# Optimization experiments

Hardware: AMD Instinct MI355X
Metric: run time of the kernel (lower is better)

The kernel has to match this reference:

```python
import jax, jax.numpy as jnp
import numpy as np

ROPE_THETA = 10000.0


def apply_rope(q, k, cos, sin):
    # q,k: [B,H,S,D]; cos,sin: [S,D/2] -> broadcast [1,1,S,D/2]
    def rot(t):
        t2 = t.reshape(*t.shape[:-1], -1, 2)  # [B,H,S,D/2,2]
        te, to = t2[..., 0], t2[..., 1]
        c = cos[None, None, :, :]
        s = sin[None, None, :, :]
        re = te * c - to * s
        im = te * s + to * c
        return jnp.stack([re, im], axis=-1).reshape(t.shape)
    return rot(q), rot(k)


def setup_inputs() -> dict:
    key = jax.random.key(0)
    ks = jax.random.split(key, 4)
    B, S, D, H = 2, 2048, 1024, 16
    hd = D // H
    x = jax.random.normal(ks[0], (B, S, D), dtype=jnp.float32)
    # causal boolean mask (True = keep)
    mask = jnp.tril(jnp.ones((S, S), dtype=bool))[None, None]
    # rotary tables
    inv_freq = 1.0 / (ROPE_THETA ** (jnp.arange(0, hd, 2, dtype=jnp.float32) / hd))  # [hd/2]
    t = jnp.arange(S, dtype=jnp.float32)
    ang = t[:, None] * inv_freq[None, :]  # [S, hd/2]
    freqs_cos = jnp.cos(ang)
    freqs_sin = jnp.sin(ang)
    W_qkv = jax.random.normal(ks[1], (D, 3 * D), dtype=jnp.float32) * 0.02
    b_qkv = jnp.zeros((3 * D,), dtype=jnp.float32)
    W_o = jax.random.normal(ks[2], (D, D), dtype=jnp.float32) * 0.02
    b_o = jnp.zeros((D,), dtype=jnp.float32)
    return {"x": x, "mask": mask, "freqs_cos": freqs_cos, "freqs_sin": freqs_sin,
            "W_qkv": W_qkv, "b_qkv": b_qkv, "W_o": W_o, "b_o": b_o}


def reference(x, mask, freqs_cos, freqs_sin, W_qkv, b_qkv, W_o, b_o):
    B, S, D = x.shape
    H = 16
    hd = D // H
    scale = hd ** -0.5
    qkv = x @ W_qkv + b_qkv  # [B,S,3D]
    q, k, v = jnp.split(qkv, 3, axis=-1)
    q = q.reshape(B, S, H, hd).transpose(0, 2, 1, 3)  # [B,H,S,hd]
    k = k.reshape(B, S, H, hd).transpose(0, 2, 1, 3)
    v = v.reshape(B, S, H, hd).transpose(0, 2, 1, 3)
    q, k = apply_rope(q, k, freqs_cos, freqs_sin)
    scores = jnp.einsum('bhqd,bhkd->bhqk', q, k) * scale
    scores = jnp.where(mask, scores, jnp.finfo(scores.dtype).min)
    attn = jax.nn.softmax(scores, axis=-1)
    out = jnp.einsum('bhqk,bhkd->bhqd', attn, v)
    out = out.transpose(0, 2, 1, 3).reshape(B, S, D)
    return out @ W_o + b_o
```

## Files before the change

kernel.cpp:

```cpp
#include <hip/hip_runtime.h>
#include <hip/hip_bf16.h>
#include <stdint.h>

typedef unsigned short u16;
typedef __attribute__((ext_vector_type(8))) __bf16 bf16x8;
typedef __attribute__((ext_vector_type(4))) float f32x4;
typedef __attribute__((ext_vector_type(16))) float f32x16;
typedef __attribute__((ext_vector_type(8))) u16 u16x8;

__device__ __forceinline__ u16 f2bf(float f) {
  union { float f; unsigned int u; } v; v.f = f;
  unsigned int r = v.u + 0x7fffu + ((v.u >> 16) & 1u);
  return (u16)(r >> 16);
}
__device__ __forceinline__ unsigned pack2(float lo, float hi) {
  return (unsigned)f2bf(lo) | ((unsigned)f2bf(hi) << 16);
}

__device__ __forceinline__ f32x4 mfma16(bf16x8 a, bf16x8 b, f32x4 c) {
  return __builtin_amdgcn_mfma_f32_16x16x32_bf16(a, b, c, 0, 0, 0);
}
__device__ __forceinline__ f32x16 mfma32(bf16x8 a, bf16x8 b, f32x16 c) {
  return __builtin_amdgcn_mfma_f32_32x32x16_bf16(a, b, c, 0, 0, 0);
}

__device__ __forceinline__ void gload16(const void* g, void* l) {
  __builtin_amdgcn_global_load_lds((const __attribute__((address_space(1))) void*)g,
                                   (__attribute__((address_space(3))) void*)l,
                                   16, 0, 0);
}

__global__ void cast_bf16_kernel(const float* __restrict__ in, u16* __restrict__ out, int n) {
  int i = (blockIdx.x * 256 + threadIdx.x) * 8;
  if (i >= n) return;
  const float4* p = (const float4*)(in + i);
  float4 a = p[0], b = p[1];
  u16x8 o;
  o[0] = f2bf(a.x); o[1] = f2bf(a.y); o[2] = f2bf(a.z); o[3] = f2bf(a.w);
  o[4] = f2bf(b.x); o[5] = f2bf(b.y); o[6] = f2bf(b.z); o[7] = f2bf(b.w);
  *(u16x8*)(out + i) = o;
}

__global__ void transpose_cast_k(const float* __restrict__ in, u16* __restrict__ out,
                                 int R, int Ccols) {
  __shared__ float tile[64][65];
  const int c0 = (int)blockIdx.x << 6, r0 = (int)blockIdx.y << 6;
  const int tx = threadIdx.x & 63, ty = threadIdx.x >> 6;
#pragma unroll
  for (int i = ty; i < 64; i += 4)
    tile[i][tx] = in[(size_t)(r0 + i) * Ccols + c0 + tx];
  __syncthreads();
#pragma unroll
  for (int i = ty; i < 64; i += 4)
    out[(size_t)(c0 + i) * R + r0 + tx] = f2bf(tile[tx][i]);
}

__global__ __launch_bounds__(256, 3)
void gemm_qkv(const u16* __restrict__ A, const u16* __restrict__ Bt,
              const float* __restrict__ bias,
              const float* __restrict__ fc, const float* __restrict__ fs,
              u16* __restrict__ qr, u16* __restrict__ kr, u16* __restrict__ vr) {
  const int K = 1024;
  __shared__ __align__(16) u16 smem[128 * 136];
  u16* const As = smem;
  u16* const Bs = smem + 8192;
  const int m0 = (int)(blockIdx.x / 24) << 7;
  const int n0 = (int)(blockIdx.x % 24) << 7;
  const int tid = threadIdx.x;
  const int l = tid & 63, lg = l >> 4, ll = l & 15;
  const int w = tid >> 6;
  const int wr = (w >> 1) << 6, wc = (w & 1) << 6;
  const int srow = tid >> 2, scol = (tid & 3) << 3;
  const u16* ga = A + (size_t)(m0 + srow) * K + scol;
  const u16* gb = Bt + (size_t)(n0 + srow) * K + scol;
  const size_t K64 = (size_t)64 * K;
  u16* const la00 = &As[srow * 32 + scol];
  u16* const la01 = &As[4096 + srow * 32 + scol];
  u16* const la10 = &As[(srow + 64) * 32 + scol];
  u16* const la11 = &As[4096 + (srow + 64) * 32 + scol];
  u16* const lb00 = &Bs[srow * 32 + scol];
  u16* const lb01 = &Bs[4096 + srow * 32 + scol];
  u16* const lb10 = &Bs[(srow + 64) * 32 + scol];
  u16* const lb11 = &Bs[4096 + (srow + 64) * 32 + scol];
  f32x4 acc[4][4] = {};
  for (int kt = 0; kt < K; kt += 64) {
    gload16(ga + kt, la00);       gload16(ga + kt + 32, la01);
    gload16(ga + kt + K64, la10); gload16(ga + kt + K64 + 32, la11);
    gload16(gb + kt, lb00);       gload16(gb + kt + 32, lb01);
    gload16(gb + kt + K64, lb10); gload16(gb + kt + K64 + 32, lb11);
    __syncthreads();
#pragma unroll
    for (int h = 0; h < 2; ++h) {
      bf16x8 a[4], b[4];
#pragma unroll
      for (int i = 0; i < 4; ++i) {
        a[i] = *(const bf16x8*)&As[h * 4096 + (wr + i * 16 + ll) * 32 + lg * 8];
        b[i] = *(const bf16x8*)&Bs[h * 4096 + (wc + i * 16 + ll) * 32 + lg * 8];
      }
#pragma unroll
      for (int mi = 0; mi < 4; ++mi)
#pragma unroll
        for (int ni = 0; ni < 4; ++ni)
          acc[mi][ni] = mfma16(a[mi], b[ni], acc[mi][ni]);
    }
    __syncthreads();
  }
  const int sec = n0 >> 10;
  u16* const dst = (sec == 0) ? qr : (sec == 1) ? kr : vr;
  const int h0 = (n0 & 1023) >> 6;
#pragma unroll
  for (int ni = 0; ni < 4; ++ni) {
    const int cc = wc + ni * 16 + ll;
    const int n = n0 + cc;
    const int d = n & 63;
    const float bi_ = bias[n];
    const int i2 = d >> 1;
    const bool odd = d & 1;
#pragma unroll
    for (int mi = 0; mi < 4; ++mi) {
#pragma unroll
      for (int r = 0; r < 4; ++r) {
        const int rr = wr + mi * 16 + lg * 4 + r;
        const int s = (m0 + rr) & 2047;
        float v = acc[mi][ni][r] + bi_;
        if (sec < 2) {
          const float c = fc[s * 32 + i2], sn = fs[s * 32 + i2];
          const float p = __shfl_xor(v, 1);
          v = odd ? (p * sn + v * c) : (v * c - p * sn);
          if (sec == 0) v *= 0.125f;
        }
        smem[rr * 136 + cc] = f2bf(v);
      }
    }
  }
  __syncthreads();
#pragma unroll
  for (int it = 0; it < 8; ++it) {
    const int c = it * 256 + tid;
    const int j = c & 7, hh = (c >> 3) & 1, rr = c >> 4;
    const int row = m0 + rr;
    const int bb = row >> 11, ss = row & 2047;
    const uint4 val = *(const uint4*)&smem[rr * 136 + hh * 64 + j * 8];
    *(uint4*)&dst[((size_t)(((bb << 4) + h0 + hh) << 11) + ss) * 64 + j * 8] = val;
  }
}

__global__ __launch_bounds__(256, 2)
void gemm_bt(const u16* __restrict__ A, const u16* __restrict__ Bt,
             const float* __restrict__ bias, float* __restrict__ C,
             int M, int N, int K) {
  __shared__ __align__(16) u16 As[2 * 128 * 32];
  __shared__ __align__(16) u16 Bs[2 * 128 * 32];
  const int nb = N >> 7;
  const int m0 = (int)(blockIdx.x / nb) << 7;
  const int n0 = (int)(blockIdx.x % nb) << 7;
  const int tid = threadIdx.x;
  const int l = tid & 63, lg = l >> 4, ll = l & 15;
  const int w = tid >> 6;
  const int wr = (w >> 1) << 6, wc = (w & 1) << 6;
  const int srow = tid >> 2, scol = (tid & 3) << 3;
  const u16* ga = A + (size_t)(m0 + srow) * K + scol;
  const u16* gb = Bt + (size_t)(n0 + srow) * K + scol;
  const size_t K64 = (size_t)64 * K;
  u16* const la00 = &As[srow * 32 + scol];
  u16* const la01 = &As[4096 + srow * 32 + scol];
  u16* const la10 = &As[(srow + 64) * 32 + scol];
  u16* const la11 = &As[4096 + (srow + 64) * 32 + scol];
  u16* const lb00 = &Bs[srow * 32 + scol];
  u16* const lb01 = &Bs[4096 + srow * 32 + scol];
  u16* const lb10 = &Bs[(srow + 64) * 32 + scol];
  u16* const lb11 = &Bs[4096 + (srow + 64) * 32 + scol];
  f32x4 acc[4][4] = {};
  for (int kt = 0; kt < K; kt += 64) {
    gload16(ga + kt, la00);       gload16(ga + kt + 32, la01);
    gload16(ga + kt + K64, la10); gload16(ga + kt + K64 + 32, la11);
    gload16(gb + kt, lb00);       gload16(gb + kt + 32, lb01);
    gload16(gb + kt + K64, lb10); gload16(gb + kt + K64 + 32, lb11);
    __syncthreads();
#pragma unroll
    for (int h = 0; h < 2; ++h) {
      bf16x8 a[4], b[4];
#pragma unroll
      for (int i = 0; i < 4; ++i) {
        a[i] = *(const bf16x8*)&As[h * 4096 + (wr + i * 16 + ll) * 32 + lg * 8];
        b[i] = *(const bf16x8*)&Bs[h * 4096 + (wc + i * 16 + ll) * 32 + lg * 8];
      }
#pragma unroll
      for (int mi = 0; mi < 4; ++mi)
#pragma unroll
        for (int ni = 0; ni < 4; ++ni)
          acc[mi][ni] = mfma16(a[mi], b[ni], acc[mi][ni]);
    }
    __syncthreads();
  }
#pragma unroll
  for (int mi = 0; mi < 4; ++mi) {
#pragma unroll
    for (int r = 0; r < 4; ++r) {
      const int row = m0 + wr + mi * 16 + lg * 4 + r;
      float* crow = C + (size_t)row * N + n0 + wc;
#pragma unroll
      for (int ni = 0; ni < 4; ++ni)
        crow[ni * 16 + ll] = acc[mi][ni][r] + bias[n0 + wc + ni * 16 + ll];
    }
  }
}

__global__ void v_transpose_bf16(const u16* __restrict__ vr, u16* __restrict__ vtc) {
  __shared__ u16 tile[64][66];
  const int bh = blockIdx.x;
  const int s0 = (int)blockIdx.y << 6;
  const int tx = threadIdx.x & 63, ty = threadIdx.x >> 6;
#pragma unroll
  for (int i = ty; i < 64; i += 4)
    tile[i][tx] = vr[((size_t)bh * 2048 + s0 + i) * 64 + tx];
  __syncthreads();
  u16* const outc = vtc + ((size_t)bh * 32 + (s0 >> 6)) * 4096;
#pragma unroll
  for (int i = ty; i < 64; i += 4)
    outc[i * 64 + tx] = tile[tx][i];
}

__global__ __launch_bounds__(256, 2)
void attn_k(const u16* __restrict__ qr, const u16* __restrict__ kr,
            const u16* __restrict__ vtc, u16* __restrict__ aout) {
  __shared__ __align__(16) char kvlds[16384];
  const int bi = (int)blockIdx.x;
  const int bh = bi & 31;
  const int qt = (bi < 256) ? (15 - (bi >> 5)) : ((bi - 256) >> 5);
  const int tid = threadIdx.x;
  const int w = tid >> 6, l = tid & 63, hi = l >> 5, ql = l & 31;
  const u16* Q  = qr + (size_t)bh * (2048 * 64);
  const u16* Kp = kr + (size_t)bh * (2048 * 64);
  const int q0w = (qt << 7) + (w << 5);
  const int qg = q0w + ql;
  bf16x8 qf[4];
#pragma unroll
  for (int mi = 0; mi < 4; ++mi)
    qf[mi] = *(const bf16x8*)&Q[(size_t)qg * 64 + mi * 16 + hi * 8];
  const int sr = tid >> 2, sc = (tid & 3) * 32;
  const int wo0 = (sr * 128 + sc) ^ ((sr & 7) << 4);
  const int wo1 = (sr * 128 + sc + 16) ^ ((sr & 7) << 4);
  const char* kga = (const char*)(Kp + (size_t)sr * 64) + sc;
  const char* vga = (const char*)(vtc + (size_t)bh * 32 * 4096) + sr * 128 + sc;
  const int swz = (ql & 7) << 4;
  f32x16 oa = {}, ob = {};
  float mrow = -1e30f, lp = 0.f;
  const int nch = 2 * qt + 2;
  uint4 sk0 = *(const uint4*)(kga), sk1 = *(const uint4*)(kga + 16);
  uint4 sv0 = *(const uint4*)(vga), sv1 = *(const uint4*)(vga + 16);
  for (int ch = 0; ch < nch; ++ch) {
    asm volatile("s_waitcnt vmcnt(0)" ::: "memory");
    asm volatile("s_barrier" ::: "memory");
    *(uint4*)(kvlds + wo0) = sk0;
    *(uint4*)(kvlds + wo1) = sk1;
    *(uint4*)(kvlds + 8192 + wo0) = sv0;
    *(uint4*)(kvlds + 8192 + wo1) = sv1;
    if (ch + 1 < nch) {
      const size_t kof = (size_t)(ch + 1) * 8192;
      sk0 = *(const uint4*)(kga + kof); sk1 = *(const uint4*)(kga + kof + 16);
      sv0 = *(const uint4*)(vga + kof); sv1 = *(const uint4*)(vga + kof + 16);
    }
    asm volatile("s_waitcnt lgkmcnt(0)" ::: "memory");
    asm volatile("s_barrier" ::: "memory");
    const int kb = ch << 6;
    if (kb > q0w + 31) continue;
    f32x16 s0 = {}, s1 = {};
#pragma unroll
    for (int mi = 0; mi < 4; ++mi) {
      const int cb = mi * 32 + hi * 16;
      const bf16x8 k0 = *(const bf16x8*)(kvlds + ((ql * 128 + cb) ^ swz));
      const bf16x8 k1 = *(const bf16x8*)(kvlds + (((32 + ql) * 128 + cb) ^ swz));
      s0 = mfma32(k0, qf[mi], s0);
      s1 = mfma32(k1, qf[mi], s1);
    }
    if (kb + 63 > q0w) {
#pragma unroll
      for (int r = 0; r < 16; ++r) {
        const int kvo = (r & 3) + 8 * (r >> 2) + 4 * hi;
        if (kb + kvo > qg) s0[r] = -1e30f;
        if (kb + 32 + kvo > qg) s1[r] = -1e30f;
      }
    }
    float mx = s0[0];
#pragma unroll
    for (int r = 1; r < 16; ++r) mx = fmaxf(mx, s0[r]);
#pragma unroll
    for (int r = 0; r < 16; ++r) mx = fmaxf(mx, s1[r]);
    mx = fmaxf(mx, __shfl_xor(mx, 32));
    if (!__all(mx <= mrow + 8.f)) {
      const float mn = fmaxf(mrow, mx);
      const float esc = __expf(mrow - mn);
      mrow = mn;
      lp *= esc;
#pragma unroll
      for (int r = 0; r < 16; ++r) { oa[r] *= esc; ob[r] *= esc; }
    }
    float p0[16], p1[16];
#pragma unroll
    for (int r = 0; r < 16; ++r) {
      p0[r] = __expf(s0[r] - mrow);
      p1[r] = __expf(s1[r] - mrow);
      lp += p0[r] + p1[r];
    }
    bf16x8 pb[4];
#pragma unroll
    for (int s = 0; s < 2; ++s) {
      const float* ps = s ? p1 : p0;
#pragma unroll
      for (int j = 0; j < 2; ++j) {
        const unsigned X0 = pack2(ps[j * 8 + 0], ps[j * 8 + 1]);
        const unsigned X1 = pack2(ps[j * 8 + 2], ps[j * 8 + 3]);
        const unsigned Y0 = pack2(ps[j * 8 + 4], ps[j * 8 + 5]);
        const unsigned Y1 = pack2(ps[j * 8 + 6], ps[j * 8 + 7]);
        const unsigned sX0 = (unsigned)__shfl_xor((int)X0, 32);
        const unsigned sX1 = (unsigned)__shfl_xor((int)X1, 32);
        const unsigned sY0 = (unsigned)__shfl_xor((int)Y0, 32);
        const unsigned sY1 = (unsigned)__shfl_xor((int)Y1, 32);
        union { unsigned u[4]; bf16x8 v; } t;
        t.u[0] = hi ? sY0 : X0;
        t.u[1] = hi ? sY1 : X1;
        t.u[2] = hi ? Y0 : sX0;
        t.u[3] = hi ? Y1 : sX1;
        pb[s * 2 + j] = t.v;
      }
    }
#pragma unroll
    for (int jj = 0; jj < 4; ++jj) {
      const int cb = jj * 32 + hi * 16;
      const bf16x8 va = *(const bf16x8*)(kvlds + 8192 + ((ql * 128 + cb) ^ swz));
      const bf16x8 vb = *(const bf16x8*)(kvlds + 8192 + (((32 + ql) * 128 + cb) ^ swz));
      oa = mfma32(va, pb[jj], oa);
      ob = mfma32(vb, pb[jj], ob);
    }
  }
  lp += __shfl_xor(lp, 32);
  const float inv = 1.0f / lp;
  const int hcol = (bh & 15) << 6;
  const int tok = ((bh >> 4) << 11) + qg;
  unsigned* orow = (unsigned*)(aout + (size_t)tok * 1024 + hcol);
#pragma unroll
  for (int r = 0; r < 16; r += 2) {
    const int d0 = (r & 3) + 8 * (r >> 2) + 4 * hi;
    orow[d0 >> 1]        = pack2(oa[r] * inv, oa[r + 1] * inv);
    orow[(32 + d0) >> 1] = pack2(ob[r] * inv, ob[r + 1] * inv);
  }
}

extern "C" void kernel_launch(void* const* d_in, const int* in_sizes, int n_in,
                              void* d_out, int out_size, void* d_ws, size_t ws_size,
                              hipStream_t stream) {
  const float* x    = (const float*)d_in[0];
  const float* fc   = (const float*)d_in[2];
  const float* fs   = (const float*)d_in[3];
  const float* Wqkv = (const float*)d_in[4];
  const float* bqkv = (const float*)d_in[5];
  const float* Wo   = (const float*)d_in[6];
  const float* bo   = (const float*)d_in[7];
  float* out = (float*)d_out;

  size_t off = 0;
  auto alloc = [&](size_t bytes) {
    void* p = (char*)d_ws + off;
    off += (bytes + 255) & ~(size_t)255;
    return p;
  };
  u16*   xb   = (u16*)  alloc(4096ull * 1024 * 2);
  u16*   wqt  = (u16*)  alloc(3072ull * 1024 * 2);
  u16*   wot  = (u16*)  alloc(1024ull * 1024 * 2);
  u16*   qr_  = (u16*)  alloc(32ull * 2048 * 64 * 2);
  u16*   kr_  = (u16*)  alloc(32ull * 2048 * 64 * 2);
  u16*   vr_  = (u16*)  alloc(32ull * 2048 * 64 * 2);
  u16*   vtc_ = (u16*)  alloc(32ull * 32 * 4096 * 2);
  u16*   ao_  = (u16*)  alloc(4096ull * 1024 * 2);

  cast_bf16_kernel<<<2048, 256, 0, stream>>>(x, xb, 4096 * 1024);
  transpose_cast_k<<<dim3(48, 16), 256, 0, stream>>>(Wqkv, wqt, 1024, 3072);
  transpose_cast_k<<<dim3(16, 16), 256, 0, stream>>>(Wo, wot, 1024, 1024);
  gemm_qkv<<<dim3(32 * 24), 256, 0, stream>>>(xb, wqt, bqkv, fc, fs, qr_, kr_, vr_);
  v_transpose_bf16<<<dim3(32, 32), 256, 0, stream>>>(vr_, vtc_);
  attn_k<<<dim3(512), 256, 0, stream>>>(qr_, kr_, vtc_, ao_);
  gemm_bt<<<dim3(32 * 8), 256, 0, stream>>>(ao_, wot, bo, out, 4096, 1024, 1024);
}
```

Before: 133.4 us.

## Double-buffer K/V tiles in LDS and skip fully masked half-tiles

Splits the attention kernel's shared memory into two K/V buffers. The next chunk is written to LDS while the current one is consumed, which drops one barrier and the vmcnt wait per iteration. It also skips the upper 32-key QK^T MFMAs, their exp work and the matching PV MFMAs when that half-tile is entirely above the causal diagonal. Instruction priority is raised around the MFMA sections. LDS use doubles to 32KB per block, which may limit occupancy with two blocks per CU.

Measured after the change: 137.6 us. 1.03x slower.

```diff
diff --git a/kernel.cpp b/kernel.cpp
--- a/kernel.cpp
+++ b/kernel.cpp
@@ -224,7 +224,7 @@
 __global__ __launch_bounds__(256, 2)
 void attn_k(const u16* __restrict__ qr, const u16* __restrict__ kr,
             const u16* __restrict__ vtc, u16* __restrict__ aout) {
-  __shared__ __align__(16) char kvlds[16384];
+  __shared__ __align__(16) char kvlds[2][16384];
   const int bi = (int)blockIdx.x;
   const int bh = bi & 31;
   const int qt = (bi < 256) ? (15 - (bi >> 5)) : ((bi - 256) >> 5);
@@ -249,90 +249,126 @@
   const int nch = 2 * qt + 2;
   uint4 sk0 = *(const uint4*)(kga), sk1 = *(const uint4*)(kga + 16);
   uint4 sv0 = *(const uint4*)(vga), sv1 = *(const uint4*)(vga + 16);
+  *(uint4*)(kvlds[0] + wo0) = sk0;
+  *(uint4*)(kvlds[0] + wo1) = sk1;
+  *(uint4*)(kvlds[0] + 8192 + wo0) = sv0;
+  *(uint4*)(kvlds[0] + 8192 + wo1) = sv1;
+  sk0 = *(const uint4*)(kga + 8192); sk1 = *(const uint4*)(kga + 8192 + 16);
+  sv0 = *(const uint4*)(vga + 8192); sv1 = *(const uint4*)(vga + 8192 + 16);
+  asm volatile("s_waitcnt lgkmcnt(0)" ::: "memory");
+  asm volatile("s_barrier" ::: "memory");
   for (int ch = 0; ch < nch; ++ch) {
-    asm volatile("s_waitcnt vmcnt(0)" ::: "memory");
-    asm volatile("s_barrier" ::: "memory");
-    *(uint4*)(kvlds + wo0) = sk0;
-    *(uint4*)(kvlds + wo1) = sk1;
-    *(uint4*)(kvlds + 8192 + wo0) = sv0;
-    *(uint4*)(kvlds + 8192 + wo1) = sv1;
+    const int cur = ch & 1;
+    const char* kbuf = kvlds[cur];
+    const char* vbuf = kbuf + 8192;
+    char* const nbuf = kvlds[cur ^ 1];
     if (ch + 1 < nch) {
-      const size_t kof = (size_t)(ch + 1) * 8192;
-      sk0 = *(const uint4*)(kga + kof); sk1 = *(const uint4*)(kga + kof + 16);
-      sv0 = *(const uint4*)(vga + kof); sv1 = *(const uint4*)(vga + kof + 16);
+      *(uint4*)(nbuf + wo0) = sk0;
+      *(uint4*)(nbuf + wo1) = sk1;
+      *(uint4*)(nbuf + 8192 + wo0) = sv0;
+      *(uint4*)(nbuf + 8192 + wo1) = sv1;
+      if (ch + 2 < nch) {
+        const size_t of = (size_t)(ch + 2) * 8192;
+        sk0 = *(const uint4*)(kga + of); sk1 = *(const uint4*)(kga + of + 16);
+        sv0 = *(const uint4*)(vga + of); sv1 = *(const uint4*)(vga + of + 16);
+      }
+    }
+    const int kb = ch << 6;
+    if (kb <= q0w + 31) {
+      const bool dohi = (kb + 32) <= (q0w + 31);
+      f32x16 s0 = {}, s1 = {};
+      __builtin_amdgcn_s_setprio(1);
+#pragma unroll
+      for (int mi = 0; mi < 4; ++mi) {
+        const int cb = mi * 32 + hi * 16;
+        const bf16x8 k0 = *(const bf16x8*)(kbuf + ((ql * 128 + cb) ^ swz));
+        s0 = mfma32(k0, qf[mi], s0);
+      }
+      if (dohi) {
+#pragma unroll
+        for (int mi = 0; mi < 4; ++mi) {
+          const int cb = mi * 32 + hi * 16;
+          const bf16x8 k1 = *(const bf16x8*)(kbuf + (((32 + ql) * 128 + cb) ^ swz));
+          s1 = mfma32(k1, qf[mi], s1);
+        }
+      }
+      __builtin_amdgcn_s_setprio(0);
+      if (kb + 63 > q0w) {
+#pragma unroll
+        for (int r = 0; r < 16; ++r) {
+          const int kvo = (r & 3) + 8 * (r >> 2) + 4 * hi;
+          if (kb + kvo > qg) s0[r] = -1e30f;
+          if (kb + 32 + kvo > qg) s1[r] = -1e30f;
+        }
+      }
+      float mx = s0[0];
+#pragma unroll
+      for (int r = 1; r < 16; ++r) mx = fmaxf(mx, s0[r]);
+      if (dohi) {
+#pragma unroll
+        for (int r = 0; r < 16; ++r) mx = fmaxf(mx, s1[r]);
+      }
+      mx = fmaxf(mx, __shfl_xor(mx, 32));
+      if (!__all(mx <= mrow + 8.f)) {
+        const float mn = fmaxf(mrow, mx);
+        const float esc = __expf(mrow - mn);
+        mrow = mn;
+        lp *= esc;
+#pragma unroll
+        for (int r = 0; r < 16; ++r) { oa[r] *= esc; ob[r] *= esc; }
+      }
+      float p0[16], p1[16];
+#pragma unroll
+      for (int r = 0; r < 16; ++r) {
+        p0[r] = __expf(s0[r] - mrow);
+        lp += p0[r];
+      }
+      if (dohi) {
+#pragma unroll
+        for (int r = 0; r < 16; ++r) {
+          p1[r] = __expf(s1[r] - mrow);
+          lp += p1[r];
+        }
+      }
+      bf16x8 pb[4];
+      const int nseg = dohi ? 2 : 1;
+#pragma unroll
+      for (int s = 0; s < 2; ++s) {
+        if (s >= nseg) break;
+        const float* ps = s ? p1 : p0;
+#pragma unroll
+        for (int j = 0; j < 2; ++j) {
+          const unsigned X0 = pack2(ps[j * 8 + 0], ps[j * 8 + 1]);
+          const unsigned X1 = pack2(ps[j * 8 + 2], ps[j * 8 + 3]);
+          const unsigned Y0 = pack2(ps[j * 8 + 4], ps[j * 8 + 5]);
+          const unsigned Y1 = pack2(ps[j * 8 + 6], ps[j * 8 + 7]);
+          const unsigned sX0 = (unsigned)__shfl_xor((int)X0, 32);
+          const unsigned sX1 = (unsigned)__shfl_xor((int)X1, 32);
+          const unsigned sY0 = (unsigned)__shfl_xor((int)Y0, 32);
+          const unsigned sY1 = (unsigned)__shfl_xor((int)Y1, 32);
+          union { unsigned u[4]; bf16x8 v; } t;
+          t.u[0] = hi ? sY0 : X0;
+          t.u[1] = hi ? sY1 : X1;
+          t.u[2] = hi ? Y0 : sX0;
+          t.u[3] = hi ? Y1 : sX1;
+          pb[s * 2 + j] = t.v;
+        }
+      }
+      const int njj = dohi ? 4 : 2;
+      __builtin_amdgcn_s_setprio(1);
+#pragma unroll
+      for (int jj = 0; jj < 4; ++jj) {
+        if (jj >= njj) break;
+        const int cb = jj * 32 + hi * 16;
+        const bf16x8 va = *(const bf16x8*)(vbuf + ((ql * 128 + cb) ^ swz));
+        const bf16x8 vb = *(const bf16x8*)(vbuf + (((32 + ql) * 128 + cb) ^ swz));
+        oa = mfma32(va, pb[jj], oa);
+        ob = mfma32(vb, pb[jj], ob);
+      }
+      __builtin_amdgcn_s_setprio(0);
     }
     asm volatile("s_waitcnt lgkmcnt(0)" ::: "memory");
     asm volatile("s_barrier" ::: "memory");
-    const int kb = ch << 6;
-    if (kb > q0w + 31) continue;
-    f32x16 s0 = {}, s1 = {};
-#pragma unroll
-    for (int mi = 0; mi < 4; ++mi) {
-      const int cb = mi * 32 + hi * 16;
-      const bf16x8 k0 = *(const bf16x8*)(kvlds + ((ql * 128 + cb) ^ swz));
-      const bf16x8 k1 = *(const bf16x8*)(kvlds + (((32 + ql) * 128 + cb) ^ swz));
-      s0 = mfma32(k0, qf[mi], s0);
-      s1 = mfma32(k1, qf[mi], s1);
-    }
-    if (kb + 63 > q0w) {
-#pragma unroll
-      for (int r = 0; r < 16; ++r) {
-        const int kvo = (r & 3) + 8 * (r >> 2) + 4 * hi;
-        if (kb + kvo > qg) s0[r] = -1e30f;
-        if (kb + 32 + kvo > qg) s1[r] = -1e30f;
-      }
-    }
-    float mx = s0[0];
-#pragma unroll
-    for (int r = 1; r < 16; ++r) mx = fmaxf(mx, s0[r]);
-#pragma unroll
-    for (int r = 0; r < 16; ++r) mx = fmaxf(mx, s1[r]);
-    mx = fmaxf(mx, __shfl_xor(mx, 32));
-    if (!__all(mx <= mrow + 8.f)) {
-      const float mn = fmaxf(mrow, mx);
-      const float esc = __expf(mrow - mn);
-      mrow = mn;
-      lp *= esc;
-#pragma unroll
-      for (int r = 0; r < 16; ++r) { oa[r] *= esc; ob[r] *= esc; }
-    }
-    float p0[16], p1[16];
-#pragma unroll
-    for (int r = 0; r < 16; ++r) {
-      p0[r] = __expf(s0[r] - mrow);
-      p1[r] = __expf(s1[r] - mrow);
-      lp += p0[r] + p1[r];
-    }
-    bf16x8 pb[4];
-#pragma unroll
-    for (int s = 0; s < 2; ++s) {
-      const float* ps = s ? p1 : p0;
-#pragma unroll
-      for (int j = 0; j < 2; ++j) {
-        const unsigned X0 = pack2(ps[j * 8 + 0], ps[j * 8 + 1]);
-        const unsigned X1 = pack2(ps[j * 8 + 2], ps[j * 8 + 3]);
-        const unsigned Y0 = pack2(ps[j * 8 + 4], ps[j * 8 + 5]);
-        const unsigned Y1 = pack2(ps[j * 8 + 6], ps[j * 8 + 7]);
-        const unsigned sX0 = (unsigned)__shfl_xor((int)X0, 32);
-        const unsigned sX1 = (unsigned)__shfl_xor((int)X1, 32);
-        const unsigned sY0 = (unsigned)__shfl_xor((int)Y0, 32);
-        const unsigned sY1 = (unsigned)__shfl_xor((int)Y1, 32);
-        union { unsigned u[4]; bf16x8 v; } t;
-        t.u[0] = hi ? sY0 : X0;
-        t.u[1] = hi ? sY1 : X1;
-        t.u[2] = hi ? Y0 : sX0;
-        t.u[3] = hi ? Y1 : sX1;
-        pb[s * 2 + j] = t.v;
-      }
-    }
-#pragma unroll
-    for (int jj = 0; jj < 4; ++jj) {
-      const int cb = jj * 32 + hi * 16;
-      const bf16x8 va = *(const bf16x8*)(kvlds + 8192 + ((ql * 128 + cb) ^ swz));
-      const bf16x8 vb = *(const bf16x8*)(kvlds + 8192 + (((32 + ql) * 128 + cb) ^ swz));
-      oa = mfma32(va, pb[jj], oa);
-      ob = mfma32(vb, pb[jj], ob);
-    }
   }
   lp += __shfl_xor(lp, 32);
   const float inv = 1.0f / lp;
```

## Split long causal query tiles across two blocks with a separate softmax merge kernel

Applied to the files above, without the earlier changes.

The eight longest query tiles of each head (rows 1024-2047) are now split along the key dimension into two halves, each handled by its own block. The halves write unnormalized fp32 partial outputs plus running max and sum to workspace, and a new merge kernel combines them with rescaling. This balances per-block work under the causal mask and raises the grid from 512 to 768 blocks to cut tail latency. The cost is one extra launch and the fp32 round trip of the partial results through global memory.

Result: slower. 138.6 us (+3.9%).

```diff
diff --git a/kernel.cpp b/kernel.cpp
--- a/kernel.cpp
+++ b/kernel.cpp
@@ -223,11 +223,28 @@
 
 __global__ __launch_bounds__(256, 2)
 void attn_k(const u16* __restrict__ qr, const u16* __restrict__ kr,
-            const u16* __restrict__ vtc, u16* __restrict__ aout) {
+            const u16* __restrict__ vtc, u16* __restrict__ aout,
+            float* __restrict__ pO, float* __restrict__ pML) {
   __shared__ __align__(16) char kvlds[16384];
   const int bi = (int)blockIdx.x;
   const int bh = bi & 31;
-  const int qt = (bi < 256) ? (15 - (bi >> 5)) : ((bi - 256) >> 5);
+  const int sidx = bi >> 5;
+  int qt, ch0, ch1, half;
+  bool split;
+  if (sidx < 16) {
+    qt = 15 - (sidx >> 1);
+    half = sidx & 1;
+    split = true;
+    const int hc = qt + 1;
+    ch0 = half ? hc : 0;
+    ch1 = half ? (2 * qt + 2) : hc;
+  } else {
+    qt = 23 - sidx;
+    half = 0;
+    split = false;
+    ch0 = 0;
+    ch1 = 2 * qt + 2;
+  }
   const int tid = threadIdx.x;
   const int w = tid >> 6, l = tid & 63, hi = l >> 5, ql = l & 31;
   const u16* Q  = qr + (size_t)bh * (2048 * 64);
@@ -246,17 +263,18 @@
   const int swz = (ql & 7) << 4;
   f32x16 oa = {}, ob = {};
   float mrow = -1e30f, lp = 0.f;
-  const int nch = 2 * qt + 2;
-  uint4 sk0 = *(const uint4*)(kga), sk1 = *(const uint4*)(kga + 16);
-  uint4 sv0 = *(const uint4*)(vga), sv1 = *(const uint4*)(vga + 16);
-  for (int ch = 0; ch < nch; ++ch) {
+  uint4 sk0 = *(const uint4*)(kga + (size_t)ch0 * 8192);
+  uint4 sk1 = *(const uint4*)(kga + (size_t)ch0 * 8192 + 16);
+  uint4 sv0 = *(const uint4*)(vga + (size_t)ch0 * 8192);
+  uint4 sv1 = *(const uint4*)(vga + (size_t)ch0 * 8192 + 16);
+  for (int ch = ch0; ch < ch1; ++ch) {
     asm volatile("s_waitcnt vmcnt(0)" ::: "memory");
     asm volatile("s_barrier" ::: "memory");
     *(uint4*)(kvlds + wo0) = sk0;
     *(uint4*)(kvlds + wo1) = sk1;
     *(uint4*)(kvlds + 8192 + wo0) = sv0;
     *(uint4*)(kvlds + 8192 + wo1) = sv1;
-    if (ch + 1 < nch) {
+    if (ch + 1 < ch1) {
       const size_t kof = (size_t)(ch + 1) * 8192;
       sk0 = *(const uint4*)(kga + kof); sk1 = *(const uint4*)(kga + kof + 16);
       sv0 = *(const uint4*)(vga + kof); sv1 = *(const uint4*)(vga + kof + 16);
@@ -335,16 +353,49 @@
     }
   }
   lp += __shfl_xor(lp, 32);
-  const float inv = 1.0f / lp;
+  if (!split) {
+    const float inv = 1.0f / lp;
+    const int hcol = (bh & 15) << 6;
+    const int tok = ((bh >> 4) << 11) + qg;
+    unsigned* orow = (unsigned*)(aout + (size_t)tok * 1024 + hcol);
+#pragma unroll
+    for (int r = 0; r < 16; r += 2) {
+      const int d0 = (r & 3) + 8 * (r >> 2) + 4 * hi;
+      orow[d0 >> 1]        = pack2(oa[r] * inv, oa[r + 1] * inv);
+      orow[(32 + d0) >> 1] = pack2(ob[r] * inv, ob[r + 1] * inv);
+    }
+  } else {
+    const int ridx = (bh << 10) + (qg - 1024);
+    float* prow = pO + ((size_t)ridx * 2 + half) * 64;
+#pragma unroll
+    for (int r = 0; r < 16; r += 2) {
+      const int d0 = (r & 3) + 8 * (r >> 2) + 4 * hi;
+      *(float2*)&prow[d0]      = make_float2(oa[r], oa[r + 1]);
+      *(float2*)&prow[32 + d0] = make_float2(ob[r], ob[r + 1]);
+    }
+    if (hi == 0) {
+      pML[((size_t)ridx * 2 + half) * 2 + 0] = mrow;
+      pML[((size_t)ridx * 2 + half) * 2 + 1] = lp;
+    }
+  }
+}
+
+__global__ void attn_merge(const float* __restrict__ pO, const float* __restrict__ pML,
+                           u16* __restrict__ aout) {
+  const int idx = (int)blockIdx.x * 256 + threadIdx.x;
+  const int d = idx & 63;
+  const int rr = idx >> 6;
+  const float mA = pML[rr * 4 + 0], lA = pML[rr * 4 + 1];
+  const float mB = pML[rr * 4 + 2], lB = pML[rr * 4 + 3];
+  const float M = fmaxf(mA, mB);
+  const float eA = __expf(mA - M), eB = __expf(mB - M);
+  const float num = pO[((size_t)rr * 2 + 0) * 64 + d] * eA
+                  + pO[((size_t)rr * 2 + 1) * 64 + d] * eB;
+  const float den = lA * eA + lB * eB;
+  const int bh = rr >> 10, row = (rr & 1023) + 1024;
+  const int tok = ((bh >> 4) << 11) + row;
   const int hcol = (bh & 15) << 6;
-  const int tok = ((bh >> 4) << 11) + qg;
-  unsigned* orow = (unsigned*)(aout + (size_t)tok * 1024 + hcol);
-#pragma unroll
-  for (int r = 0; r < 16; r += 2) {
-    const int d0 = (r & 3) + 8 * (r >> 2) + 4 * hi;
-    orow[d0 >> 1]        = pack2(oa[r] * inv, oa[r + 1] * inv);
-    orow[(32 + d0) >> 1] = pack2(ob[r] * inv, ob[r + 1] * inv);
-  }
+  aout[(size_t)tok * 1024 + hcol + d] = f2bf(num / den);
 }
 
 extern "C" void kernel_launch(void* const* d_in, const int* in_sizes, int n_in,
@@ -373,12 +424,15 @@
   u16*   vr_  = (u16*)  alloc(32ull * 2048 * 64 * 2);
   u16*   vtc_ = (u16*)  alloc(32ull * 32 * 4096 * 2);
   u16*   ao_  = (u16*)  alloc(4096ull * 1024 * 2);
+  float* pO_  = (float*)alloc(32ull * 1024 * 2 * 64 * 4);
+  float* pML_ = (float*)alloc(32ull * 1024 * 2 * 2 * 4);
 
   cast_bf16_kernel<<<2048, 256, 0, stream>>>(x, xb, 4096 * 1024);
   transpose_cast_k<<<dim3(48, 16), 256, 0, stream>>>(Wqkv, wqt, 1024, 3072);
   transpose_cast_k<<<dim3(16, 16), 256, 0, stream>>>(Wo, wot, 1024, 1024);
   gemm_qkv<<<dim3(32 * 24), 256, 0, stream>>>(xb, wqt, bqkv, fc, fs, qr_, kr_, vr_);
   v_transpose_bf16<<<dim3(32, 32), 256, 0, stream>>>(vr_, vtc_);
-  attn_k<<<dim3(512), 256, 0, stream>>>(qr_, kr_, vtc_, ao_);
+  attn_k<<<dim3(768), 256, 0, stream>>>(qr_, kr_, vtc_, ao_, pO_, pML_);
+  attn_merge<<<dim3(8192), 256, 0, stream>>>(pO_, pML_, ao_);
   gemm_bt<<<dim3(32 * 8), 256, 0, stream>>>(ao_, wot, bo, out, 4096, 1024, 1024);
 }
```
